# Kernel optimization log

Hardware: AMD Instinct MI355X
Metric: run time of the kernel (lower is better)

The kernel has to match this reference:

```python
import jax, jax.numpy as jnp
import numpy as np

D, H, O, E, K = 512, 2048, 512, 8, 2
CF = 1.0  # capacity_factor


def setup_inputs() -> dict:
    key = jax.random.key(0)
    ks = jax.random.split(key, 4)
    s = lambda k, shape, sc: jax.random.normal(k, shape, jnp.float32) * sc
    return {
        "x": s(ks[0], (8, 2048, D), 1.0),
        "gate_w": s(ks[1], (D, E), D ** -0.5),
        "gate_b": jnp.zeros((E,), jnp.float32),
        "w1": s(ks[2], (E, D, H), D ** -0.5),
        "b1": jnp.zeros((E, H), jnp.float32),
        "w2": s(ks[3], (E, H, O), H ** -0.5),
        "b2": jnp.zeros((E, O), jnp.float32),
    }


def _moe(x, gate_w, gate_b, w1, b1, w2, b2):
    orig = x.shape
    xf = x.reshape(-1, orig[-1])            # [N, D]
    N = xf.shape[0]
    capacity = max(int((N / E) * CF), 4)    # static (shape-derived)

    logits = xf @ gate_w + gate_b           # [N, E]
    gate_probs = jax.nn.softmax(logits, axis=-1)
    topk_p, topk_i = jax.lax.top_k(gate_probs, K)          # [N, K]
    norm_p = topk_p / topk_p.sum(-1, keepdims=True)        # [N, K]

    hot = jax.nn.one_hot(topk_i, E, dtype=xf.dtype)        # [N, K, E]
    mask = hot.sum(1)                                      # [N, E] in {0,1} (top-k indices unique)
    w_te = (norm_p[..., None] * hot).sum(1)                # [N, E] routing weight per token/expert

    def dispatch(m):
        # m: [N] 0/1 mask for one expert; keep first `capacity` tokens in token order
        cs = jnp.cumsum(m)
        keep = (m > 0) & (cs <= capacity)
        idx = jnp.argsort(jnp.where(keep, 0, 1), stable=True)[:capacity]  # kept tokens first, in order
        valid = jnp.arange(capacity) < keep.sum()
        return idx, valid

    idx, valid = jax.vmap(dispatch)(mask.T)                # idx: [E, cap], valid: [E, cap]

    gathered = xf[idx]                                     # [E, cap, D]
    h = jax.nn.gelu(jnp.einsum('ecd,edh->ech', gathered, w1) + b1[:, None, :], approximate=False)
    out = jnp.einsum('ech,eho->eco', h, w2) + b2[:, None, :]  # [E, cap, O]

    wg = w_te[idx, jnp.arange(E)[:, None]]                 # [E, cap] gate weight per dispatched token
    contrib = out * (wg * valid.astype(out.dtype))[..., None]
    combined = jnp.zeros((N, O), out.dtype).at[idx.reshape(-1)].add(contrib.reshape(-1, O))
    return combined.reshape(*orig[:-1], O), gate_probs


def reference(x, gate_w, gate_b, w1, b1, w2, b2):
    return _moe(x, gate_w, gate_b, w1, b1, w2, b2)
```

## Files before the change

### kernel.cpp

```cpp
#include <hip/hip_runtime.h>
#include <hip/hip_bf16.h>

#define NTOK 16384
#define DDIM 512
#define HDIM 2048
#define ODIM 512
#define NE 8
#define CAP 2048

typedef __attribute__((ext_vector_type(8))) short short8v;
typedef __attribute__((ext_vector_type(4))) short short4v;
typedef __attribute__((ext_vector_type(8))) unsigned short ushort8v;
typedef __attribute__((ext_vector_type(4))) float f32x4;

static __device__ __forceinline__ unsigned short f2bf(float f) {
  __hip_bfloat16 h = __float2bfloat16(f);
  return __builtin_bit_cast(unsigned short, h);
}

#define GLOAD_LDS16(gp, lp)                                               \
  __builtin_amdgcn_global_load_lds(                                       \
      (const __attribute__((address_space(1))) void*)(gp),                \
      (__attribute__((address_space(3))) void*)(lp), 16, 0, 0)

__device__ __forceinline__ void transpose_block(const float* __restrict__ src,
                                                __hip_bfloat16* __restrict__ dst,
                                                int R, int C, int b) {
  __shared__ float tile[32][33];
  int nx = C >> 5, ny = R >> 5;
  int x = b % nx, y = (b / nx) % ny, e = b / (nx * ny);
  size_t base = (size_t)e * R * C;
  int c0 = x * 32, r0 = y * 32;
  int tx = threadIdx.x & 31, ty = threadIdx.x >> 5;
#pragma unroll
  for (int i = 0; i < 32; i += 8)
    tile[ty + i][tx] = src[base + (size_t)(r0 + ty + i) * C + c0 + tx];
  __syncthreads();
#pragma unroll
  for (int i = 0; i < 32; i += 8)
    dst[base + (size_t)(c0 + ty + i) * R + r0 + tx] = __float2bfloat16(tile[tx][ty + i]);
}

__global__ void k_prep(const float* __restrict__ x, const float* __restrict__ gw,
                       const float* __restrict__ gb, const float* __restrict__ w1,
                       __hip_bfloat16* __restrict__ w1t, const float* __restrict__ w2,
                       __hip_bfloat16* __restrict__ w2t, float* __restrict__ gate_probs,
                       int2* __restrict__ tk_e, float2* __restrict__ tk_w,
                       int* __restrict__ token_slot) {
  int b = blockIdx.x;
  if (b < 8192) { transpose_block(w1, w1t, DDIM, HDIM, b); return; }
  if (b < 16384) { transpose_block(w2, w2t, HDIM, ODIM, b - 8192); return; }
  b -= 16384;
  __shared__ float gws[DDIM * 9];
  int tid = threadIdx.x;
  for (int i = tid; i < DDIM * NE; i += 256) {
    int d = i >> 3, e = i & 7;
    gws[d * 9 + e] = gw[i];
  }
  __syncthreads();
  int wid = tid >> 6, lane = tid & 63;
  int t = b * 4 + wid;
  const float* xr = x + (size_t)t * DDIM;
  float acc[NE] = {0.f, 0.f, 0.f, 0.f, 0.f, 0.f, 0.f, 0.f};
#pragma unroll
  for (int j = 0; j < 8; ++j) {
    float xv = xr[lane + 64 * j];
    const float* g = &gws[(lane + 64 * j) * 9];
#pragma unroll
    for (int e = 0; e < NE; ++e) acc[e] += xv * g[e];
  }
#pragma unroll
  for (int e = 0; e < NE; ++e) {
#pragma unroll
    for (int off = 32; off > 0; off >>= 1) acc[e] += __shfl_xor(acc[e], off, 64);
  }
  if (lane == 0) {
    float p[NE];
    float m = -1e30f;
#pragma unroll
    for (int e = 0; e < NE; ++e) { p[e] = acc[e] + gb[e]; m = fmaxf(m, p[e]); }
    float s = 0.f;
#pragma unroll
    for (int e = 0; e < NE; ++e) { p[e] = expf(p[e] - m); s += p[e]; }
    float inv = 1.f / s;
#pragma unroll
    for (int e = 0; e < NE; ++e) { p[e] *= inv; gate_probs[(size_t)t * NE + e] = p[e]; }
    int i1 = 0; float p1 = p[0];
#pragma unroll
    for (int e = 1; e < NE; ++e) if (p[e] > p1) { p1 = p[e]; i1 = e; }
    int i2 = -1; float p2 = -1e30f;
#pragma unroll
    for (int e = 0; e < NE; ++e) if (e != i1 && p[e] > p2) { p2 = p[e]; i2 = e; }
    float wsum = p1 + p2;
    tk_e[t] = make_int2(i1, i2);
    tk_w[t] = make_float2(p1 / wsum, p2 / wsum);
    token_slot[2 * t] = -1;
    token_slot[2 * t + 1] = -1;
  }
}

__global__ void k_dispatch(const int2* __restrict__ tk_e, int* __restrict__ token_slot,
                           int* __restrict__ expert_tokens) {
  int e = blockIdx.x;
  int tid = threadIdx.x;
  int lane = tid & 63, w = tid >> 6;
  __shared__ int wave_cnt[16];
  int base = 0;
  for (int chunk = 0; chunk < NTOK / 1024; ++chunk) {
    int t = chunk * 1024 + tid;
    int2 te = tk_e[t];
    int k = (te.x == e) ? 0 : ((te.y == e) ? 1 : -1);
    bool flag = (k >= 0);
    unsigned long long m = __ballot(flag);
    int pre = __popcll(m & ((1ull << lane) - 1ull));
    __syncthreads();
    if (lane == 0) wave_cnt[w] = __popcll(m);
    __syncthreads();
    int off = 0, total = 0;
#pragma unroll
    for (int i = 0; i < 16; ++i) {
      off += (i < w) ? wave_cnt[i] : 0;
      total += wave_cnt[i];
    }
    int rank = base + off + pre;
    if (flag && rank < CAP) {
      expert_tokens[e * CAP + rank] = t;
      token_slot[2 * t + k] = e * CAP + rank;
    }
    base += total;
  }
  int nvalid = base < CAP ? base : CAP;
  for (int s = nvalid + tid; s < CAP; s += 1024)
    expert_tokens[e * CAP + s] = 0;
}

__global__ void k_gather(const float* __restrict__ x,
                         const int* __restrict__ expert_tokens,
                         __hip_bfloat16* __restrict__ xg) {
  int tid = threadIdx.x, wid = tid >> 6, lane = tid & 63;
  int slot = blockIdx.x * 4 + wid;
  int tok = expert_tokens[slot];
  const float4* src = reinterpret_cast<const float4*>(x + (size_t)tok * DDIM) + lane * 2;
  float4 u = src[0], v = src[1];
  ushort8v o;
  o[0] = f2bf(u.x); o[1] = f2bf(u.y); o[2] = f2bf(u.z); o[3] = f2bf(u.w);
  o[4] = f2bf(v.x); o[5] = f2bf(v.y); o[6] = f2bf(v.z); o[7] = f2bf(v.w);
  *reinterpret_cast<ushort8v*>(xg + (size_t)slot * DDIM + lane * 8) = o;
}

static __device__ __forceinline__ float gelu_fast(float v) {
  float z = 1.5957691216057308f * (v + 0.044715f * v * v * v);
  return v / (1.f + __expf(-z));
}

template <int K, int M, bool GELU, typename OutT>
__global__ __launch_bounds__(256, 2) void k_gemm(
    const __hip_bfloat16* __restrict__ A, const __hip_bfloat16* __restrict__ B,
    const float* __restrict__ bias, OutT* __restrict__ C) {
  __shared__ char lds[2][24576];
  int gx = gridDim.x, gy = gridDim.y;
  int lin = (blockIdx.z * gy + blockIdx.y) * gx + blockIdx.x;
  int total = gx * gy * (int)gridDim.z;
  int cpx = total >> 3;
  lin = (lin & 7) * cpx + (lin >> 3);
  int gxy = gx * gy;
  int e = lin / gxy;
  int rem = lin - e * gxy;
  int mt = rem / gx, nt = rem - mt * gx;

  const int m0 = mt * 256, n0 = nt * 128;
  const int tid = threadIdx.x;
  const int lane = tid & 63, wid = tid >> 6;
  const int wr = wid >> 1, wc = wid & 1;
  const int lrow = lane & 15, kseg = lane >> 4;

  const int r0 = tid >> 2;
  const int sc = (tid & 3) ^ ((r0 >> 1) & 3);
  const int cb = (tid & 192) * 16;
  const __hip_bfloat16* Ab = A + ((size_t)e * M + m0) * K;
  const __hip_bfloat16* Bb = B + ((size_t)e * CAP + n0) * K;

#define STAGE(buf, kk)                                                           \
  do {                                                                           \
    _Pragma("unroll")                                                            \
    for (int j = 0; j < 4; ++j)                                                  \
      GLOAD_LDS16(Ab + (size_t)(r0 + 64 * j) * K + (kk) + sc * 8,                \
                  lds[buf] + j * 4096 + cb);                                     \
    _Pragma("unroll")                                                            \
    for (int j = 0; j < 2; ++j)                                                  \
      GLOAD_LDS16(Bb + (size_t)(r0 + 64 * j) * K + (kk) + sc * 8,                \
                  lds[buf] + 16384 + j * 4096 + cb);                             \
  } while (0)

#define READ_A(dst, bi, half)                                                    \
  do {                                                                           \
    _Pragma("unroll")                                                            \
    for (int mm = 0; mm < 4; ++mm) {                                             \
      int rr = wr * 128 + (half) * 64 + mm * 16 + lrow;                          \
      int ks = kseg ^ ((rr >> 1) & 3);                                           \
      dst[mm] = *reinterpret_cast<const short8v*>(lds[bi] + rr * 64 + ks * 16);  \
    }                                                                            \
  } while (0)

#define READ_B(dst, bi)                                                          \
  do {                                                                           \
    _Pragma("unroll")                                                            \
    for (int nn = 0; nn < 4; ++nn) {                                             \
      int rr = wc * 64 + nn * 16 + lrow;                                         \
      int ks = kseg ^ ((rr >> 1) & 3);                                           \
      dst[nn] = *reinterpret_cast<const short8v*>(lds[bi] + 16384 + rr * 64 +    \
                                                  ks * 16);                      \
    }                                                                            \
  } while (0)

#define MFMA_HALF(afr, half)                                                     \
  do {                                                                           \
    __builtin_amdgcn_s_setprio(1);                                               \
    _Pragma("unroll")                                                            \
    for (int mm = 0; mm < 4; ++mm)                                               \
      _Pragma("unroll")                                                          \
      for (int nn = 0; nn < 4; ++nn)                                             \
        acc[(half) * 4 + mm][nn] = __builtin_amdgcn_mfma_f32_16x16x32_bf16(      \
            afr[mm], bfr[nn], acc[(half) * 4 + mm][nn], 0, 0, 0);                \
    __builtin_amdgcn_s_setprio(0);                                               \
  } while (0)

  f32x4 acc[8][4] = {};
  short8v a0[4], a1[4], bfr[4];
  const int T = K >> 5;

  STAGE(0, 0);
  STAGE(1, 32);
  int bt = 0;
  for (int t = 0; t < T; ++t) {
    if (t < T - 1) asm volatile("s_waitcnt vmcnt(6)" ::: "memory");
    else           asm volatile("s_waitcnt vmcnt(0)" ::: "memory");
    __builtin_amdgcn_s_barrier();
    READ_A(a0, bt, 0);
    READ_B(bfr, bt);
    asm volatile("s_waitcnt lgkmcnt(0)" ::: "memory");
    __builtin_amdgcn_sched_barrier(0);
    READ_A(a1, bt, 1);
    MFMA_HALF(a0, 0);
    asm volatile("s_waitcnt lgkmcnt(0)" ::: "memory");
    __builtin_amdgcn_sched_barrier(0);
    __builtin_amdgcn_s_barrier();
    if (t + 2 < T) STAGE(bt, (t + 2) * 32);
    MFMA_HALF(a1, 1);
    bt ^= 1;
  }
#undef STAGE
#undef READ_A
#undef READ_B
#undef MFMA_HALF

#pragma unroll
  for (int half = 0; half < 2; ++half) {
#pragma unroll
    for (int mm = 0; mm < 4; ++mm) {
      int mrow = m0 + wr * 128 + half * 64 + mm * 16 + kseg * 4;
      float4 bv = *reinterpret_cast<const float4*>(&bias[e * M + mrow]);
#pragma unroll
      for (int nn = 0; nn < 4; ++nn) {
        int token = n0 + wc * 64 + nn * 16 + lrow;
        float v0 = acc[half * 4 + mm][nn][0] + bv.x;
        float v1 = acc[half * 4 + mm][nn][1] + bv.y;
        float v2 = acc[half * 4 + mm][nn][2] + bv.z;
        float v3 = acc[half * 4 + mm][nn][3] + bv.w;
        if (GELU) {
          v0 = gelu_fast(v0); v1 = gelu_fast(v1);
          v2 = gelu_fast(v2); v3 = gelu_fast(v3);
        }
        OutT* cp = C + ((size_t)e * CAP + token) * M + mrow;
        if constexpr (__is_same(OutT, __hip_bfloat16)) {
          short4v o;
          o[0] = (short)f2bf(v0); o[1] = (short)f2bf(v1);
          o[2] = (short)f2bf(v2); o[3] = (short)f2bf(v3);
          *reinterpret_cast<short4v*>(cp) = o;
        } else {
          float4 o = {v0, v1, v2, v3};
          *reinterpret_cast<float4*>(cp) = o;
        }
      }
    }
  }
}

__global__ void k_combine(const float* __restrict__ outbuf,
                          const int* __restrict__ token_slot,
                          const float2* __restrict__ tk_w,
                          float* __restrict__ comb) {
  int tid = threadIdx.x;
  int wid = tid >> 6, lane = tid & 63;
  int t = blockIdx.x * 4 + wid;
  int s0 = token_slot[2 * t], s1 = token_slot[2 * t + 1];
  float2 w = tk_w[t];
  float r[8] = {0.f, 0.f, 0.f, 0.f, 0.f, 0.f, 0.f, 0.f};
  if (s0 >= 0) {
    const float4* p = reinterpret_cast<const float4*>(outbuf + (size_t)s0 * ODIM + lane * 8);
    float4 a = p[0], b = p[1];
    r[0] += w.x * a.x; r[1] += w.x * a.y; r[2] += w.x * a.z; r[3] += w.x * a.w;
    r[4] += w.x * b.x; r[5] += w.x * b.y; r[6] += w.x * b.z; r[7] += w.x * b.w;
  }
  if (s1 >= 0) {
    const float4* p = reinterpret_cast<const float4*>(outbuf + (size_t)s1 * ODIM + lane * 8);
    float4 a = p[0], b = p[1];
    r[0] += w.y * a.x; r[1] += w.y * a.y; r[2] += w.y * a.z; r[3] += w.y * a.w;
    r[4] += w.y * b.x; r[5] += w.y * b.y; r[6] += w.y * b.z; r[7] += w.y * b.w;
  }
  float4* q = reinterpret_cast<float4*>(comb + (size_t)t * ODIM + lane * 8);
  float4 o0 = {r[0], r[1], r[2], r[3]};
  float4 o1 = {r[4], r[5], r[6], r[7]};
  q[0] = o0;
  q[1] = o1;
}

extern "C" void kernel_launch(void* const* d_in, const int* in_sizes, int n_in,
                              void* d_out, int out_size, void* d_ws, size_t ws_size,
                              hipStream_t stream) {
  const float* x      = (const float*)d_in[0];
  const float* gate_w = (const float*)d_in[1];
  const float* gate_b = (const float*)d_in[2];
  const float* w1     = (const float*)d_in[3];
  const float* b1     = (const float*)d_in[4];
  const float* w2     = (const float*)d_in[5];
  const float* b2     = (const float*)d_in[6];

  float* comb = (float*)d_out;
  float* gate_probs = comb + (size_t)NTOK * ODIM;

  char* ws = (char*)d_ws;
  __hip_bfloat16* w1t    = (__hip_bfloat16*)(ws);
  __hip_bfloat16* w2t    = (__hip_bfloat16*)(ws + 16777216);
  __hip_bfloat16* hbuf   = (__hip_bfloat16*)(ws + 33554432);
  __hip_bfloat16* xg     = (__hip_bfloat16*)(ws + 100663296);
  float*          outbuf = (float*)(ws + 100663296);
  int*   expert_tokens   = (int*)(ws + 134217728);
  int2*  tk_e            = (int2*)(ws + 134283264);
  float2* tk_w           = (float2*)(ws + 134414336);
  int*   token_slot      = (int*)(ws + 134545408);

  k_prep<<<16384 + NTOK / 4, 256, 0, stream>>>(x, gate_w, gate_b, w1, w1t, w2, w2t,
                                               gate_probs, tk_e, tk_w, token_slot);
  k_dispatch<<<NE, 1024, 0, stream>>>(tk_e, token_slot, expert_tokens);
  k_gather<<<NE * CAP / 4, 256, 0, stream>>>(x, expert_tokens, xg);
  k_gemm<DDIM, HDIM, true, __hip_bfloat16>
      <<<dim3(CAP / 128, HDIM / 256, NE), 256, 0, stream>>>(w1t, xg, b1, hbuf);
  k_gemm<HDIM, ODIM, false, float>
      <<<dim3(CAP / 128, ODIM / 256, NE), 256, 0, stream>>>(w2t, hbuf, b2, outbuf);
  k_combine<<<NTOK / 4, 256, 0, stream>>>(outbuf, token_slot, tk_w, comb);
}
```

Baseline: 174.5 us.

## Load GEMM B fragments directly from global into registers with triple-buffered LDS A

The B operand (token activations) is no longer staged through LDS. Each wave loads its B MFMA fragments straight from global memory into registers, double-buffered across k-steps. The LDS for A becomes a three-stage ring so the next-next tile can be issued before the current one is consumed, which removes one barrier per k-step. This cuts LDS traffic and synchronisation, at the cost of uncoalesced per-lane global reads for B and higher register pressure from holding 8 A fragments plus two B buffers.

```diff
diff --git a/kernel.cpp b/kernel.cpp
--- a/kernel.cpp
+++ b/kernel.cpp
@@ -157,7 +157,7 @@
 __global__ __launch_bounds__(256, 2) void k_gemm(
     const __hip_bfloat16* __restrict__ A, const __hip_bfloat16* __restrict__ B,
     const float* __restrict__ bias, OutT* __restrict__ C) {
-  __shared__ char lds[2][24576];
+  __shared__ char lds[3][16384];
   int gx = gridDim.x, gy = gridDim.y;
   int lin = (blockIdx.z * gy + blockIdx.y) * gx + blockIdx.x;
   int total = gx * gy * (int)gridDim.z;
@@ -178,109 +178,105 @@
   const int sc = (tid & 3) ^ ((r0 >> 1) & 3);
   const int cb = (tid & 192) * 16;
   const __hip_bfloat16* Ab = A + ((size_t)e * M + m0) * K;
-  const __hip_bfloat16* Bb = B + ((size_t)e * CAP + n0) * K;
-
-#define STAGE(buf, kk)                                                           \
-  do {                                                                           \
-    _Pragma("unroll")                                                            \
-    for (int j = 0; j < 4; ++j)                                                  \
-      GLOAD_LDS16(Ab + (size_t)(r0 + 64 * j) * K + (kk) + sc * 8,                \
-                  lds[buf] + j * 4096 + cb);                                     \
-    _Pragma("unroll")                                                            \
-    for (int j = 0; j < 2; ++j)                                                  \
-      GLOAD_LDS16(Bb + (size_t)(r0 + 64 * j) * K + (kk) + sc * 8,                \
-                  lds[buf] + 16384 + j * 4096 + cb);                             \
+  const char* Bbc = (const char*)(B + ((size_t)e * CAP + n0) * K);
+
+  int vB[4];
+#pragma unroll
+  for (int nn = 0; nn < 4; ++nn)
+    vB[nn] = (wc * 64 + nn * 16 + lrow) * (K * 2) + kseg * 16;
+
+#define STAGE(buf, kk)                                                        \
+  do {                                                                        \
+    _Pragma("unroll")                                                         \
+    for (int j = 0; j < 4; ++j)                                               \
+      GLOAD_LDS16(Ab + (size_t)(r0 + 64 * j) * K + (kk) + sc * 8,             \
+                  lds[buf] + j * 4096 + cb);                                  \
   } while (0)
 
-#define READ_A(dst, bi, half)                                                    \
-  do {                                                                           \
-    _Pragma("unroll")                                                            \
-    for (int mm = 0; mm < 4; ++mm) {                                             \
-      int rr = wr * 128 + (half) * 64 + mm * 16 + lrow;                          \
-      int ks = kseg ^ ((rr >> 1) & 3);                                           \
-      dst[mm] = *reinterpret_cast<const short8v*>(lds[bi] + rr * 64 + ks * 16);  \
-    }                                                                            \
+#define LOADB(dst, kt)                                                        \
+  do {                                                                        \
+    _Pragma("unroll")                                                         \
+    for (int nn = 0; nn < 4; ++nn)                                            \
+      dst[nn] = *reinterpret_cast<const short8v*>(Bbc + vB[nn] + (kt) * 64);  \
   } while (0)
 
-#define READ_B(dst, bi)                                                          \
-  do {                                                                           \
-    _Pragma("unroll")                                                            \
-    for (int nn = 0; nn < 4; ++nn) {                                             \
-      int rr = wc * 64 + nn * 16 + lrow;                                         \
-      int ks = kseg ^ ((rr >> 1) & 3);                                           \
-      dst[nn] = *reinterpret_cast<const short8v*>(lds[bi] + 16384 + rr * 64 +    \
-                                                  ks * 16);                      \
-    }                                                                            \
+#define STEP(kt, abuf, sbuf, BC, BL)                                          \
+  do {                                                                        \
+    if ((kt) < T - 1) asm volatile("s_waitcnt vmcnt(4)" ::: "memory");        \
+    else              asm volatile("s_waitcnt vmcnt(0)" ::: "memory");        \
+    __builtin_amdgcn_s_barrier();                                             \
+    _Pragma("unroll")                                                         \
+    for (int mm = 0; mm < 8; ++mm) {                                          \
+      int rr = wr * 128 + mm * 16 + lrow;                                     \
+      int ks = kseg ^ ((rr >> 1) & 3);                                        \
+      a[mm] = *reinterpret_cast<const short8v*>(lds[abuf] + rr * 64 + ks * 16); \
+    }                                                                         \
+    if ((kt) + 1 < T) LOADB(BL, (kt) + 1);                                    \
+    if ((kt) + 2 < T) STAGE(sbuf, ((kt) + 2) * 32);                           \
+    asm volatile("s_waitcnt lgkmcnt(4)" ::: "memory");                        \
+    __builtin_amdgcn_sched_barrier(0);                                        \
+    __builtin_amdgcn_s_setprio(1);                                            \
+    _Pragma("unroll")                                                         \
+    for (int mm = 0; mm < 4; ++mm)                                            \
+      _Pragma("unroll")                                                       \
+      for (int nn = 0; nn < 4; ++nn)                                          \
+        acc[mm][nn] = __builtin_amdgcn_mfma_f32_16x16x32_bf16(                \
+            a[mm], BC[nn], acc[mm][nn], 0, 0, 0);                             \
+    asm volatile("s_waitcnt lgkmcnt(0)" ::: "memory");                        \
+    __builtin_amdgcn_sched_barrier(0);                                        \
+    _Pragma("unroll")                                                         \
+    for (int mm = 4; mm < 8; ++mm)                                            \
+      _Pragma("unroll")                                                       \
+      for (int nn = 0; nn < 4; ++nn)                                          \
+        acc[mm][nn] = __builtin_amdgcn_mfma_f32_16x16x32_bf16(                \
+            a[mm], BC[nn], acc[mm][nn], 0, 0, 0);                             \
+    __builtin_amdgcn_s_setprio(0);                                            \
   } while (0)
 
-#define MFMA_HALF(afr, half)                                                     \
-  do {                                                                           \
-    __builtin_amdgcn_s_setprio(1);                                               \
-    _Pragma("unroll")                                                            \
-    for (int mm = 0; mm < 4; ++mm)                                               \
-      _Pragma("unroll")                                                          \
-      for (int nn = 0; nn < 4; ++nn)                                             \
-        acc[(half) * 4 + mm][nn] = __builtin_amdgcn_mfma_f32_16x16x32_bf16(      \
-            afr[mm], bfr[nn], acc[(half) * 4 + mm][nn], 0, 0, 0);                \
-    __builtin_amdgcn_s_setprio(0);                                               \
-  } while (0)
-
   f32x4 acc[8][4] = {};
-  short8v a0[4], a1[4], bfr[4];
+  short8v a[8], bp[4], bq[4];
   const int T = K >> 5;
 
   STAGE(0, 0);
+  LOADB(bp, 0);
   STAGE(1, 32);
+
   int bt = 0;
-  for (int t = 0; t < T; ++t) {
-    if (t < T - 1) asm volatile("s_waitcnt vmcnt(6)" ::: "memory");
-    else           asm volatile("s_waitcnt vmcnt(0)" ::: "memory");
-    __builtin_amdgcn_s_barrier();
-    READ_A(a0, bt, 0);
-    READ_B(bfr, bt);
-    asm volatile("s_waitcnt lgkmcnt(0)" ::: "memory");
-    __builtin_amdgcn_sched_barrier(0);
-    READ_A(a1, bt, 1);
-    MFMA_HALF(a0, 0);
-    asm volatile("s_waitcnt lgkmcnt(0)" ::: "memory");
-    __builtin_amdgcn_sched_barrier(0);
-    __builtin_amdgcn_s_barrier();
-    if (t + 2 < T) STAGE(bt, (t + 2) * 32);
-    MFMA_HALF(a1, 1);
-    bt ^= 1;
-  }
+  for (int t = 0; t < T; t += 2) {
+    int u1 = (bt == 2) ? 0 : bt + 1;
+    int u2 = (u1 == 2) ? 0 : u1 + 1;
+    STEP(t, bt, u2, bp, bq);
+    STEP(t + 1, u1, bt, bq, bp);
+    bt = u2;
+  }
+#undef STEP
+#undef LOADB
 #undef STAGE
-#undef READ_A
-#undef READ_B
-#undef MFMA_HALF
-
-#pragma unroll
-  for (int half = 0; half < 2; ++half) {
-#pragma unroll
-    for (int mm = 0; mm < 4; ++mm) {
-      int mrow = m0 + wr * 128 + half * 64 + mm * 16 + kseg * 4;
-      float4 bv = *reinterpret_cast<const float4*>(&bias[e * M + mrow]);
-#pragma unroll
-      for (int nn = 0; nn < 4; ++nn) {
-        int token = n0 + wc * 64 + nn * 16 + lrow;
-        float v0 = acc[half * 4 + mm][nn][0] + bv.x;
-        float v1 = acc[half * 4 + mm][nn][1] + bv.y;
-        float v2 = acc[half * 4 + mm][nn][2] + bv.z;
-        float v3 = acc[half * 4 + mm][nn][3] + bv.w;
-        if (GELU) {
-          v0 = gelu_fast(v0); v1 = gelu_fast(v1);
-          v2 = gelu_fast(v2); v3 = gelu_fast(v3);
-        }
-        OutT* cp = C + ((size_t)e * CAP + token) * M + mrow;
-        if constexpr (__is_same(OutT, __hip_bfloat16)) {
-          short4v o;
-          o[0] = (short)f2bf(v0); o[1] = (short)f2bf(v1);
-          o[2] = (short)f2bf(v2); o[3] = (short)f2bf(v3);
-          *reinterpret_cast<short4v*>(cp) = o;
-        } else {
-          float4 o = {v0, v1, v2, v3};
-          *reinterpret_cast<float4*>(cp) = o;
-        }
+
+#pragma unroll
+  for (int mm = 0; mm < 8; ++mm) {
+    int mrow = m0 + wr * 128 + mm * 16 + kseg * 4;
+    float4 bv = *reinterpret_cast<const float4*>(&bias[e * M + mrow]);
+#pragma unroll
+    for (int nn = 0; nn < 4; ++nn) {
+      int token = n0 + wc * 64 + nn * 16 + lrow;
+      float v0 = acc[mm][nn][0] + bv.x;
+      float v1 = acc[mm][nn][1] + bv.y;
+      float v2 = acc[mm][nn][2] + bv.z;
+      float v3 = acc[mm][nn][3] + bv.w;
+      if (GELU) {
+        v0 = gelu_fast(v0); v1 = gelu_fast(v1);
+        v2 = gelu_fast(v2); v3 = gelu_fast(v3);
+      }
+      OutT* cp = C + ((size_t)e * CAP + token) * M + mrow;
+      if constexpr (__is_same(OutT, __hip_bfloat16)) {
+        short4v o;
+        o[0] = (short)f2bf(v0); o[1] = (short)f2bf(v1);
+        o[2] = (short)f2bf(v2); o[3] = (short)f2bf(v3);
+        *reinterpret_cast<short4v*>(cp) = o;
+      } else {
+        float4 o = {v0, v1, v2, v3};
+        *reinterpret_cast<float4*>(cp) = o;
       }
     }
   }
```

New measurement: 217.3 us. 1.25x slower.

## Switch expert GEMMs to 256x256 tiles with 8 waves and quarter-phase pipelining

Applied to the files above, without the earlier changes.

Replaces the 256x128-tile, 4-wave GEMM with a 256x256-tile, 8-wave kernel that uses a 64-wide K step and 128 KB of LDS double buffering. Each K tile is split into four MFMA quarters, and the next tile's A/B halves are staged into LDS between them with barriers. The larger tile is meant to raise arithmetic intensity and cut global traffic per FLOP. The cost is fewer blocks per GEMM (fewer than the CU count for the second GEMM), likely one block per CU because of the LDS footprint, and more barriers per iteration.

```diff
diff --git a/kernel.cpp b/kernel.cpp
--- a/kernel.cpp
+++ b/kernel.cpp
@@ -154,10 +154,11 @@
 }
 
 template <int K, int M, bool GELU, typename OutT>
-__global__ __launch_bounds__(256, 2) void k_gemm(
+__global__ __launch_bounds__(512, 2) void k_gemm8(
     const __hip_bfloat16* __restrict__ A, const __hip_bfloat16* __restrict__ B,
     const float* __restrict__ bias, OutT* __restrict__ C) {
-  __shared__ char lds[2][24576];
+  __shared__ char lds[131072];
+  constexpr int T = K / 64;
   int gx = gridDim.x, gy = gridDim.y;
   int lin = (blockIdx.z * gy + blockIdx.y) * gx + blockIdx.x;
   int total = gx * gy * (int)gridDim.z;
@@ -168,119 +169,169 @@
   int rem = lin - e * gxy;
   int mt = rem / gx, nt = rem - mt * gx;
 
-  const int m0 = mt * 256, n0 = nt * 128;
+  const int m0 = mt * 256, n0 = nt * 256;
   const int tid = threadIdx.x;
   const int lane = tid & 63, wid = tid >> 6;
-  const int wr = wid >> 1, wc = wid & 1;
+  const int wm = wid >> 2, wn = wid & 3;
   const int lrow = lane & 15, kseg = lane >> 4;
 
-  const int r0 = tid >> 2;
-  const int sc = (tid & 3) ^ ((r0 >> 1) & 3);
-  const int cb = (tid & 192) * 16;
+  const int srow8 = tid >> 3;
+  const int ssl = (tid & 7) ^ ((tid >> 3) & 7);
   const __hip_bfloat16* Ab = A + ((size_t)e * M + m0) * K;
   const __hip_bfloat16* Bb = B + ((size_t)e * CAP + n0) * K;
 
-#define STAGE(buf, kk)                                                           \
-  do {                                                                           \
-    _Pragma("unroll")                                                            \
-    for (int j = 0; j < 4; ++j)                                                  \
-      GLOAD_LDS16(Ab + (size_t)(r0 + 64 * j) * K + (kk) + sc * 8,                \
-                  lds[buf] + j * 4096 + cb);                                     \
-    _Pragma("unroll")                                                            \
-    for (int j = 0; j < 2; ++j)                                                  \
-      GLOAD_LDS16(Bb + (size_t)(r0 + 64 * j) * K + (kk) + sc * 8,                \
-                  lds[buf] + 16384 + j * 4096 + cb);                             \
-  } while (0)
-
-#define READ_A(dst, bi, half)                                                    \
-  do {                                                                           \
-    _Pragma("unroll")                                                            \
-    for (int mm = 0; mm < 4; ++mm) {                                             \
-      int rr = wr * 128 + (half) * 64 + mm * 16 + lrow;                          \
-      int ks = kseg ^ ((rr >> 1) & 3);                                           \
-      dst[mm] = *reinterpret_cast<const short8v*>(lds[bi] + rr * 64 + ks * 16);  \
-    }                                                                            \
-  } while (0)
-
-#define READ_B(dst, bi)                                                          \
-  do {                                                                           \
-    _Pragma("unroll")                                                            \
-    for (int nn = 0; nn < 4; ++nn) {                                             \
-      int rr = wc * 64 + nn * 16 + lrow;                                         \
-      int ks = kseg ^ ((rr >> 1) & 3);                                           \
-      dst[nn] = *reinterpret_cast<const short8v*>(lds[bi] + 16384 + rr * 64 +    \
-                                                  ks * 16);                      \
-    }                                                                            \
-  } while (0)
-
-#define MFMA_HALF(afr, half)                                                     \
-  do {                                                                           \
-    __builtin_amdgcn_s_setprio(1);                                               \
-    _Pragma("unroll")                                                            \
-    for (int mm = 0; mm < 4; ++mm)                                               \
-      _Pragma("unroll")                                                          \
-      for (int nn = 0; nn < 4; ++nn)                                             \
-        acc[(half) * 4 + mm][nn] = __builtin_amdgcn_mfma_f32_16x16x32_bf16(      \
-            afr[mm], bfr[nn], acc[(half) * 4 + mm][nn], 0, 0, 0);                \
-    __builtin_amdgcn_s_setprio(0);                                               \
+#define ST_A(tt, h, buf)                                                       \
+  do {                                                                         \
+    _Pragma("unroll")                                                          \
+    for (int j = 0; j < 2; ++j)                                                \
+      GLOAD_LDS16(Ab + (size_t)((h) * 128 + j * 64 + srow8) * K +              \
+                      (size_t)(tt) * 64 + ssl * 8,                             \
+                  lds + (buf) * 65536 + (h) * 16384 + j * 8192 + tid * 16);    \
+  } while (0)
+
+#define ST_B(tt, h, buf)                                                       \
+  do {                                                                         \
+    _Pragma("unroll")                                                          \
+    for (int j = 0; j < 2; ++j)                                                \
+      GLOAD_LDS16(Bb + (size_t)((h) * 128 + j * 64 + srow8) * K +              \
+                      (size_t)(tt) * 64 + ssl * 8,                             \
+                  lds + (buf) * 65536 + 32768 + (h) * 16384 + j * 8192 +       \
+                      tid * 16);                                               \
+  } while (0)
+
+#define READ_A(dst, buf, mh)                                                   \
+  do {                                                                         \
+    _Pragma("unroll")                                                          \
+    for (int mm = 0; mm < 4; ++mm)                                             \
+      _Pragma("unroll")                                                        \
+      for (int ks = 0; ks < 2; ++ks) {                                         \
+        int rr = wm * 128 + (mh) * 64 + mm * 16 + lrow;                        \
+        int slot = (ks * 4 + kseg) ^ (rr & 7);                                 \
+        dst[mm][ks] = *reinterpret_cast<const short8v*>(                       \
+            lds + (buf) * 65536 + rr * 128 + slot * 16);                       \
+      }                                                                        \
+  } while (0)
+
+#define READ_B(dst, buf, nh)                                                   \
+  do {                                                                         \
+    _Pragma("unroll")                                                          \
+    for (int nn = 0; nn < 2; ++nn)                                             \
+      _Pragma("unroll")                                                        \
+      for (int ks = 0; ks < 2; ++ks) {                                         \
+        int rn = wn * 64 + (nh) * 32 + nn * 16 + lrow;                         \
+        int slot = (ks * 4 + kseg) ^ (rn & 7);                                 \
+        dst[nn][ks] = *reinterpret_cast<const short8v*>(                       \
+            lds + (buf) * 65536 + 32768 + rn * 128 + slot * 16);               \
+      }                                                                        \
+  } while (0)
+
+#define MFMA_Q(Af, Bf, mh, nh)                                                 \
+  do {                                                                         \
+    _Pragma("unroll")                                                          \
+    for (int mm = 0; mm < 4; ++mm)                                             \
+      _Pragma("unroll")                                                        \
+      for (int nn = 0; nn < 2; ++nn)                                           \
+        _Pragma("unroll")                                                      \
+        for (int ks = 0; ks < 2; ++ks)                                         \
+          acc[(mh) * 4 + mm][(nh) * 2 + nn] =                                  \
+              __builtin_amdgcn_mfma_f32_16x16x32_bf16(                         \
+                  Af[mm][ks], Bf[nn][ks], acc[(mh) * 4 + mm][(nh) * 2 + nn],   \
+                  0, 0, 0);                                                    \
+  } while (0)
+
+#define PH_MID()                                                               \
+  do {                                                                         \
+    __builtin_amdgcn_s_barrier();                                              \
+    asm volatile("s_waitcnt lgkmcnt(0)" ::: "memory");                         \
+    __builtin_amdgcn_sched_barrier(0);                                         \
+  } while (0)
+
+#define TILEB(t, buf, VM)                                                      \
+  do {                                                                         \
+                                                           \
+    READ_A(Ar0, buf, 0);                                                       \
+    READ_B(Br0, buf, 0);                                                       \
+    if ((t) + 1 < T) { ST_A((t) + 1, 0, (buf) ^ 1); }                          \
+    PH_MID();                                                                  \
+    __builtin_amdgcn_s_setprio(1);                                             \
+    MFMA_Q(Ar0, Br0, 0, 0);                                                    \
+    __builtin_amdgcn_s_setprio(0);                                             \
+    __builtin_amdgcn_s_barrier();                                              \
+                                                           \
+    READ_B(Br1, buf, 1);                                                       \
+    if ((t) + 1 < T) { ST_A((t) + 1, 1, (buf) ^ 1); }                          \
+    PH_MID();                                                                  \
+    __builtin_amdgcn_s_setprio(1);                                             \
+    MFMA_Q(Ar0, Br1, 0, 1);                                                    \
+    __builtin_amdgcn_s_setprio(0);                                             \
+    __builtin_amdgcn_s_barrier();                                              \
+                                                           \
+    READ_A(Ar1, buf, 1);                                                       \
+    if ((t) + 2 < T) { ST_B((t) + 2, 0, (buf)); }                              \
+    PH_MID();                                                                  \
+    __builtin_amdgcn_s_setprio(1);                                             \
+    MFMA_Q(Ar1, Br0, 1, 0);                                                    \
+    __builtin_amdgcn_s_setprio(0);                                             \
+    __builtin_amdgcn_s_barrier();                                              \
+                                                           \
+    if ((t) + 2 < T) { ST_B((t) + 2, 1, (buf)); }                              \
+    __builtin_amdgcn_s_barrier();                                              \
+    __builtin_amdgcn_s_setprio(1);                                             \
+    MFMA_Q(Ar1, Br1, 1, 1);                                                    \
+    __builtin_amdgcn_s_setprio(0);                                             \
+    asm volatile("s_waitcnt vmcnt(" VM ")" ::: "memory");                      \
+    __builtin_amdgcn_sched_barrier(0);                                         \
+    __builtin_amdgcn_s_barrier();                                              \
   } while (0)
 
   f32x4 acc[8][4] = {};
-  short8v a0[4], a1[4], bfr[4];
-  const int T = K >> 5;
-
-  STAGE(0, 0);
-  STAGE(1, 32);
-  int bt = 0;
-  for (int t = 0; t < T; ++t) {
-    if (t < T - 1) asm volatile("s_waitcnt vmcnt(6)" ::: "memory");
-    else           asm volatile("s_waitcnt vmcnt(0)" ::: "memory");
-    __builtin_amdgcn_s_barrier();
-    READ_A(a0, bt, 0);
-    READ_B(bfr, bt);
-    asm volatile("s_waitcnt lgkmcnt(0)" ::: "memory");
-    __builtin_amdgcn_sched_barrier(0);
-    READ_A(a1, bt, 1);
-    MFMA_HALF(a0, 0);
-    asm volatile("s_waitcnt lgkmcnt(0)" ::: "memory");
-    __builtin_amdgcn_sched_barrier(0);
-    __builtin_amdgcn_s_barrier();
-    if (t + 2 < T) STAGE(bt, (t + 2) * 32);
-    MFMA_HALF(a1, 1);
-    bt ^= 1;
-  }
-#undef STAGE
+  short8v Ar0[4][2], Ar1[4][2], Br0[2][2], Br1[2][2];
+
+  ST_A(0, 0, 0); ST_A(0, 1, 0); ST_B(0, 0, 0); ST_B(0, 1, 0);
+  ST_B(1, 0, 1); ST_B(1, 1, 1);
+  asm volatile("s_waitcnt vmcnt(4)" ::: "memory");
+  __builtin_amdgcn_sched_barrier(0);
+  __builtin_amdgcn_s_barrier();
+
+  for (int i = 0; i < T / 2 - 1; ++i) {
+    TILEB(2 * i, 0, "4");
+    TILEB(2 * i + 1, 1, "4");
+  }
+  TILEB(T - 2, 0, "0");
+  TILEB(T - 1, 1, "0");
+
+#undef TILEB
+#undef PH_MID
+#undef MFMA_Q
+#undef READ_B
 #undef READ_A
-#undef READ_B
-#undef MFMA_HALF
-
-#pragma unroll
-  for (int half = 0; half < 2; ++half) {
-#pragma unroll
-    for (int mm = 0; mm < 4; ++mm) {
-      int mrow = m0 + wr * 128 + half * 64 + mm * 16 + kseg * 4;
-      float4 bv = *reinterpret_cast<const float4*>(&bias[e * M + mrow]);
-#pragma unroll
-      for (int nn = 0; nn < 4; ++nn) {
-        int token = n0 + wc * 64 + nn * 16 + lrow;
-        float v0 = acc[half * 4 + mm][nn][0] + bv.x;
-        float v1 = acc[half * 4 + mm][nn][1] + bv.y;
-        float v2 = acc[half * 4 + mm][nn][2] + bv.z;
-        float v3 = acc[half * 4 + mm][nn][3] + bv.w;
-        if (GELU) {
-          v0 = gelu_fast(v0); v1 = gelu_fast(v1);
-          v2 = gelu_fast(v2); v3 = gelu_fast(v3);
-        }
-        OutT* cp = C + ((size_t)e * CAP + token) * M + mrow;
-        if constexpr (__is_same(OutT, __hip_bfloat16)) {
-          short4v o;
-          o[0] = (short)f2bf(v0); o[1] = (short)f2bf(v1);
-          o[2] = (short)f2bf(v2); o[3] = (short)f2bf(v3);
-          *reinterpret_cast<short4v*>(cp) = o;
-        } else {
-          float4 o = {v0, v1, v2, v3};
-          *reinterpret_cast<float4*>(cp) = o;
-        }
+#undef ST_B
+#undef ST_A
+
+#pragma unroll
+  for (int mi = 0; mi < 8; ++mi) {
+    int mrow = m0 + wm * 128 + mi * 16 + kseg * 4;
+    float4 bv = *reinterpret_cast<const float4*>(&bias[e * M + mrow]);
+#pragma unroll
+    for (int ni = 0; ni < 4; ++ni) {
+      int token = n0 + wn * 64 + ni * 16 + lrow;
+      float v0 = acc[mi][ni][0] + bv.x;
+      float v1 = acc[mi][ni][1] + bv.y;
+      float v2 = acc[mi][ni][2] + bv.z;
+      float v3 = acc[mi][ni][3] + bv.w;
+      if (GELU) {
+        v0 = gelu_fast(v0); v1 = gelu_fast(v1);
+        v2 = gelu_fast(v2); v3 = gelu_fast(v3);
+      }
+      OutT* cp = C + ((size_t)e * CAP + token) * M + mrow;
+      if constexpr (__is_same(OutT, __hip_bfloat16)) {
+        short4v o;
+        o[0] = (short)f2bf(v0); o[1] = (short)f2bf(v1);
+        o[2] = (short)f2bf(v2); o[3] = (short)f2bf(v3);
+        *reinterpret_cast<short4v*>(cp) = o;
+      } else {
+        float4 o = {v0, v1, v2, v3};
+        *reinterpret_cast<float4*>(cp) = o;
       }
     }
   }
@@ -344,9 +395,9 @@
                                                gate_probs, tk_e, tk_w, token_slot);
   k_dispatch<<<NE, 1024, 0, stream>>>(tk_e, token_slot, expert_tokens);
   k_gather<<<NE * CAP / 4, 256, 0, stream>>>(x, expert_tokens, xg);
-  k_gemm<DDIM, HDIM, true, __hip_bfloat16>
-      <<<dim3(CAP / 128, HDIM / 256, NE), 256, 0, stream>>>(w1t, xg, b1, hbuf);
-  k_gemm<HDIM, ODIM, false, float>
-      <<<dim3(CAP / 128, ODIM / 256, NE), 256, 0, stream>>>(w2t, hbuf, b2, outbuf);
+  k_gemm8<DDIM, HDIM, true, __hip_bfloat16>
+      <<<dim3(CAP / 256, HDIM / 256, NE), 512, 0, stream>>>(w1t, xg, b1, hbuf);
+  k_gemm8<HDIM, ODIM, false, float>
+      <<<dim3(CAP / 256, ODIM / 256, NE), 512, 0, stream>>>(w2t, hbuf, b2, outbuf);
   k_combine<<<NTOK / 4, 256, 0, stream>>>(outbuf, token_slot, tk_w, comb);
 }
```

Result: slower. 189.6 us (+8.7%).
